# Kernel optimization log

Measured on AMD Instinct MI355X. Metric: run time of the kernel, lower is better.

## Reference

```python
import jax, jax.numpy as jnp
import numpy as np

N_LAYER = 4
N_HEAD = 16
N_EMBD = 1024
BLOCK = 1024
VOCAB = 100
TRANS = 16          # obs_dim + action_dim + 2 = 11 + 3 + 2
OBS_DIM = 11
ACT_DIM = 3
B, T = 2, 1024
VTOT = VOCAB * TRANS + 1  # token embedding rows
LN_EPS = 1e-5


def _layernorm(x, w, b):
    mu = jnp.mean(x, axis=-1, keepdims=True)
    var = jnp.var(x, axis=-1, keepdims=True)
    return (x - mu) * jax.lax.rsqrt(var + LN_EPS) * w + b


def _build_mask(t):
    # causal tril with every (joined_dim-1 mod joined_dim) column zeroed
    jd = OBS_DIM + ACT_DIM + 2  # 16
    m = jnp.tril(jnp.ones((t, t), dtype=bool))
    cols = jnp.arange(t)
    m = m & ((cols % jd) != (jd - 1))[None, :]
    return m  # [T, T] bool, True = keep


def setup_inputs() -> dict:
    key = jax.random.key(0)
    ks = jax.random.split(key, 24)
    C, L, F4 = N_EMBD, N_LAYER, 4 * N_EMBD
    g = lambda k, s: jax.random.normal(k, s, dtype=jnp.float32) * 0.02
    return {
        "tokens": jax.random.randint(ks[0], (B, T), 0, VTOT),
        "tok_emb": g(ks[1], (VTOT, C)),
        "pos_emb": g(ks[2], (1, BLOCK, C)),
        "Wq": g(ks[3], (L, C, C)), "bq": jnp.zeros((L, C), jnp.float32),
        "Wk": g(ks[4], (L, C, C)), "bk": jnp.zeros((L, C), jnp.float32),
        "Wv": g(ks[5], (L, C, C)), "bv": jnp.zeros((L, C), jnp.float32),
        "Wp": g(ks[6], (L, C, C)), "bp": jnp.zeros((L, C), jnp.float32),
        "ln1w": jnp.ones((L, C), jnp.float32), "ln1b": jnp.zeros((L, C), jnp.float32),
        "ln2w": jnp.ones((L, C), jnp.float32), "ln2b": jnp.zeros((L, C), jnp.float32),
        "W1": g(ks[7], (L, C, F4)), "b1": jnp.zeros((L, F4), jnp.float32),
        "W2": g(ks[8], (L, F4, C)), "b2": jnp.zeros((L, C), jnp.float32),
        "lnfw": jnp.ones((C,), jnp.float32), "lnfb": jnp.zeros((C,), jnp.float32),
        "head_w": g(ks[9], (TRANS, VOCAB + 1, C)),
    }


def _forward(tokens, tok_emb, pos_emb, Wq, bq, Wk, bk, Wv, bv, Wp, bp,
             ln1w, ln1b, ln2w, ln2b, W1, b1, W2, b2, lnfw, lnfb, head_w):
    b, t = tokens.shape
    C, H = N_EMBD, N_HEAD
    D = C // H
    scale = 1.0 / np.sqrt(D)
    mask = _build_mask(t)[None, None]  # [1,1,T,T]

    x = tok_emb[tokens] + pos_emb[:, :t, :]  # [B,T,C]
    for i in range(N_LAYER):
        h = _layernorm(x, ln1w[i], ln1b[i])
        q = (h @ Wq[i] + bq[i]).reshape(b, t, H, D).transpose(0, 2, 1, 3)
        k = (h @ Wk[i] + bk[i]).reshape(b, t, H, D).transpose(0, 2, 1, 3)
        v = (h @ Wv[i] + bv[i]).reshape(b, t, H, D).transpose(0, 2, 1, 3)
        att = jnp.einsum('bhtd,bhsd->bhts', q, k) * scale  # attn_bias=None => +0
        att = jnp.where(mask, att, -jnp.inf)
        att = jax.nn.softmax(att, axis=-1)
        y = jnp.einsum('bhts,bhsd->bhtd', att, v)
        y = y.transpose(0, 2, 1, 3).reshape(b, t, C)
        x = x + (y @ Wp[i] + bp[i])
        h2 = _layernorm(x, ln2w[i], ln2b[i])
        x = x + (jax.nn.gelu(h2 @ W1[i] + b1[i], approximate=False) @ W2[i] + b2[i])

    x = _layernorm(x, lnfw, lnfb)
    # pad_to_full_observation + EinLinear head
    n_pad = (TRANS - t % TRANS) % TRANS
    if n_pad:
        x = jnp.concatenate([x, jnp.zeros((b, n_pad, C), x.dtype)], axis=1)
    x_pad = x.reshape(-1, TRANS, C)                    # [b*n_states, TRANS, C]
    logits = jnp.einsum('eoi,bei->beo', head_w, x_pad)  # EinLinear, bias=False
    logits = logits.reshape(b, t + n_pad, VOCAB + 1)[:, :t]
    return logits


def reference(tokens, tok_emb, pos_emb, Wq, bq, Wk, bk, Wv, bv, Wp, bp,
              ln1w, ln1b, ln2w, ln2b, W1, b1, W2, b2, lnfw, lnfb, head_w):
    return _forward(tokens, tok_emb, pos_emb, Wq, bq, Wk, bk, Wv, bv, Wp, bp,
                    ln1w, ln1b, ln2w, ln2b, W1, b1, W2, b2, lnfw, lnfb, head_w)
```

## Files before the change

### kernel.cpp

```cpp
#include <hip/hip_runtime.h>
#include <hip/hip_bf16.h>
#include <math.h>

typedef unsigned short u16;
typedef __attribute__((ext_vector_type(8))) short short8;
typedef __attribute__((ext_vector_type(4))) float f32x4;

#define CDIM 1024
#define TDIM 1024
#define NROWS 2048
#define HEADS 16
#define HD 64
#define F4 4096

__device__ __forceinline__ u16 f2bf(float f) {
    union { float f; unsigned u; } v; v.f = f;
    unsigned r = v.u + 0x7fffu + ((v.u >> 16) & 1u);
    return (u16)(r >> 16);
}

__device__ __forceinline__ void gload_lds16(const void* g, void* lds) {
    __builtin_amdgcn_global_load_lds(
        (const __attribute__((address_space(1))) unsigned int*)g,
        (__attribute__((address_space(3))) unsigned int*)lds,
        16, 0, 0);
}

__global__ __launch_bounds__(256)
void embed_k(const int* __restrict__ tok, const float* __restrict__ te,
             const float* __restrict__ pe, float* __restrict__ X)
{
    const int row = blockIdx.x;
    const int t = row & (TDIM - 1);
    const int tk = tok[row];
    const int c = threadIdx.x * 4;
    float4 a = *reinterpret_cast<const float4*>(te + (size_t)tk * CDIM + c);
    float4 b = *reinterpret_cast<const float4*>(pe + (size_t)t * CDIM + c);
    a.x += b.x; a.y += b.y; a.z += b.z; a.w += b.w;
    *reinterpret_cast<float4*>(X + (size_t)row * CDIM + c) = a;
}

template<bool BF16OUT>
__global__ __launch_bounds__(256)
void ln_k(const float* __restrict__ X, const float* __restrict__ g,
          const float* __restrict__ be, void* __restrict__ outp)
{
    __shared__ float red[4], red2[4];
    const int row = blockIdx.x, tid = threadIdx.x;
    const float* xr = X + (size_t)row * CDIM;
    const int c = tid * 4;
    float4 xv = *reinterpret_cast<const float4*>(xr + c);
    float s  = xv.x + xv.y + xv.z + xv.w;
    float s2 = xv.x*xv.x + xv.y*xv.y + xv.z*xv.z + xv.w*xv.w;
    #pragma unroll
    for (int off = 32; off; off >>= 1) {
        s  += __shfl_xor(s, off);
        s2 += __shfl_xor(s2, off);
    }
    if ((tid & 63) == 0) { red[tid >> 6] = s; red2[tid >> 6] = s2; }
    __syncthreads();
    const float ts  = red[0] + red[1] + red[2] + red[3];
    const float ts2 = red2[0] + red2[1] + red2[2] + red2[3];
    const float mu  = ts * (1.0f / CDIM);
    const float var = ts2 * (1.0f / CDIM) - mu * mu;
    const float rs  = rsqrtf(var + 1e-5f);
    float4 gv = *reinterpret_cast<const float4*>(g + c);
    float4 bv = *reinterpret_cast<const float4*>(be + c);
    float o0 = (xv.x - mu) * rs * gv.x + bv.x;
    float o1 = (xv.y - mu) * rs * gv.y + bv.y;
    float o2 = (xv.z - mu) * rs * gv.z + bv.z;
    float o3 = (xv.w - mu) * rs * gv.w + bv.w;
    if (BF16OUT) {
        u16 tmp[4] = { f2bf(o0), f2bf(o1), f2bf(o2), f2bf(o3) };
        u16* o = (u16*)outp + (size_t)row * CDIM + c;
        *reinterpret_cast<uint2*>(o) = *reinterpret_cast<const uint2*>(tmp);
    } else {
        float4 ov = { o0, o1, o2, o3 };
        *reinterpret_cast<float4*>((float*)outp + (size_t)row * CDIM + c) = ov;
    }
}

__global__ __launch_bounds__(256)
void convT_k(const float* __restrict__ W, u16* __restrict__ Wt,
             const int K, const int N)
{
    __shared__ u16 s[64][72];
    const int k0 = blockIdx.y * 64, n0 = blockIdx.x * 64;
    const int tr = threadIdx.x >> 4, tc = (threadIdx.x & 15) * 4;
    #pragma unroll
    for (int i = 0; i < 4; ++i) {
        int r = tr + i * 16;
        float4 w = *reinterpret_cast<const float4*>(W + (size_t)(k0 + r) * N + n0 + tc);
        s[r][tc + 0] = f2bf(w.x); s[r][tc + 1] = f2bf(w.y);
        s[r][tc + 2] = f2bf(w.z); s[r][tc + 3] = f2bf(w.w);
    }
    __syncthreads();
    #pragma unroll
    for (int i = 0; i < 4; ++i) {
        int n = tr + i * 16;
        u16 tmp[4];
        #pragma unroll
        for (int e = 0; e < 4; ++e) tmp[e] = s[tc + e][n];
        *reinterpret_cast<uint2*>(Wt + (size_t)(n0 + n) * K + k0 + tc) =
            *reinterpret_cast<const uint2*>(tmp);
    }
}

template<int EPI>
__global__ __launch_bounds__(256, 2)
void gemm_bt(const u16* __restrict__ A, const u16* __restrict__ Bt,
             const float* __restrict__ bias, u16* __restrict__ outb,
             float* __restrict__ resid, u16* __restrict__ vtout,
             const int N, const int K, const int KCH)
{
    __shared__ __align__(16) u16 sA[2][2][128 * 32];
    __shared__ __align__(16) u16 sB[2][2][128 * 32];
    const int tid = threadIdx.x;
    const int lane = tid & 63, wv = tid >> 6;
    const int m0 = blockIdx.y * 128, n0 = blockIdx.x * 128;
    const int kbeg = blockIdx.z * KCH, kend = kbeg + KCH;
    const int fr = lane & 15, fq = lane >> 4;
    const int wm = wv & 1, wn = wv >> 1;
    const int srow = lane >> 2, schunk = (lane & 3) * 8;
    f32x4 acc[4][4] = {};

    auto stage = [&](int k0, int buf) {
        #pragma unroll
        for (int kk = 0; kk < 2; ++kk)
            #pragma unroll
            for (int i = 0; i < 2; ++i) {
                const int reg = i * 4 + wv;
                gload_lds16(A  + (size_t)(m0 + reg * 16 + srow) * K + k0 + kk * 32 + schunk,
                            &sA[buf][kk][reg * 512]);
                gload_lds16(Bt + (size_t)(n0 + reg * 16 + srow) * K + k0 + kk * 32 + schunk,
                            &sB[buf][kk][reg * 512]);
            }
    };

    stage(kbeg, 0);
    int cur = 0;
    for (int k0 = kbeg; k0 < kend; k0 += 64) {
        __syncthreads();
        if (k0 + 64 < kend) stage(k0 + 64, cur ^ 1);
        #pragma unroll
        for (int kk = 0; kk < 2; ++kk) {
            short8 af[4], bf[4];
            #pragma unroll
            for (int mi = 0; mi < 4; ++mi)
                af[mi] = *reinterpret_cast<const short8*>(
                    &sA[cur][kk][(wm * 64 + mi * 16 + fr) * 32 + fq * 8]);
            #pragma unroll
            for (int nj = 0; nj < 4; ++nj)
                bf[nj] = *reinterpret_cast<const short8*>(
                    &sB[cur][kk][(wn * 64 + nj * 16 + fr) * 32 + fq * 8]);
            #pragma unroll
            for (int mi = 0; mi < 4; ++mi)
                #pragma unroll
                for (int nj = 0; nj < 4; ++nj)
                    acc[mi][nj] = __builtin_amdgcn_mfma_f32_16x16x32_bf16(af[mi], bf[nj], acc[mi][nj], 0, 0, 0);
        }
        cur ^= 1;
    }

    #pragma unroll
    for (int nj = 0; nj < 4; ++nj) {
        const int col = n0 + wn * 64 + nj * 16 + fr;
        const float bias_v = (EPI == 2 && blockIdx.z != 0) ? 0.0f : bias[col];
        #pragma unroll
        for (int mi = 0; mi < 4; ++mi) {
            const int rowb = m0 + wm * 64 + mi * 16 + fq * 4;
            if (EPI == 0 && vtout != nullptr && col >= 2048) {
                const int bidx = rowb >> 10, t = rowb & 1023, hd = col - 2048;
                u16 t4[4];
                #pragma unroll
                for (int r = 0; r < 4; ++r) t4[r] = f2bf(acc[mi][nj][r] + bias_v);
                *reinterpret_cast<uint2*>(
                    vtout + ((size_t)(bidx * 16 + (hd >> 6)) * 64 + (hd & 63)) * 1024 + t) =
                    *reinterpret_cast<const uint2*>(t4);
            } else {
                #pragma unroll
                for (int r = 0; r < 4; ++r) {
                    const int row = rowb + r;
                    float cv = acc[mi][nj][r] + bias_v;
                    if (EPI == 0) {
                        outb[(size_t)row * N + col] = f2bf(cv);
                    } else if (EPI == 1) {
                        float gl = 0.5f * cv * (1.0f + erff(cv * 0.70710678118654752f));
                        outb[(size_t)row * N + col] = f2bf(gl);
                    } else {
                        atomicAdd(&resid[(size_t)row * N + col], cv);
                    }
                }
            }
        }
    }
}

__global__ __launch_bounds__(256)
void attn_k(const u16* __restrict__ QKV, const u16* __restrict__ VT,
            u16* __restrict__ Y)
{
    __shared__ __align__(16) u16 sQ[64][72];
    __shared__ __align__(16) u16 sK[2][64][72];
    __shared__ __align__(16) u16 sV[2][64][72];
    __shared__ __align__(16) u16 sP[64][72];
    const int tid = threadIdx.x, lane = tid & 63, wv = tid >> 6;
    const int fr = lane & 15, fq = lane >> 4;
    const int qt = gridDim.x - 1 - blockIdx.x;
    const int h = blockIdx.y, b = blockIdx.z, q0 = qt * 64;
    const u16* Qb = QKV + (size_t)b * TDIM * 3072 + h * HD;
    const u16* Vb = VT + ((size_t)(b * HEADS + h) * HD) * TDIM;
    const int r0 = tid >> 3, c0 = (tid & 7) * 8;

    #pragma unroll
    for (int i = 0; i < 2; ++i) {
        const int r = r0 + i * 32;
        *reinterpret_cast<uint4*>(&sQ[r][c0]) =
            *reinterpret_cast<const uint4*>(Qb + (size_t)(q0 + r) * 3072 + c0);
        *reinterpret_cast<uint4*>(&sK[0][r][c0]) =
            *reinterpret_cast<const uint4*>(Qb + 1024 + (size_t)r * 3072 + c0);
        *reinterpret_cast<uint4*>(&sV[0][r][c0]) =
            *reinterpret_cast<const uint4*>(Vb + (size_t)r * TDIM + c0);
    }
    __syncthreads();

    short8 ones;
    #pragma unroll
    for (int e = 0; e < 8; ++e) ones[e] = (short)0x3F80;

    short8 aQ0 = *reinterpret_cast<const short8*>(&sQ[wv * 16 + fr][fq * 8]);
    short8 aQ1 = *reinterpret_cast<const short8*>(&sQ[wv * 16 + fr][32 + fq * 8]);
    f32x4 o[4] = {};
    f32x4 osum = {};

    for (int st = 0; st <= qt; ++st) {
        const int cur = st & 1, s0 = st * 64;
        const bool pf = st < qt;
        uint4 pk[2], pv[2];
        if (pf) {
            #pragma unroll
            for (int i = 0; i < 2; ++i) {
                const int r = r0 + i * 32;
                pk[i] = *reinterpret_cast<const uint4*>(Qb + 1024 + (size_t)(s0 + 64 + r) * 3072 + c0);
                pv[i] = *reinterpret_cast<const uint4*>(Vb + (size_t)r * TDIM + s0 + 64 + c0);
            }
        }
        f32x4 sacc[4] = {};
        #pragma unroll
        for (int j = 0; j < 4; ++j) {
            short8 b0 = *reinterpret_cast<const short8*>(&sK[cur][j * 16 + fr][fq * 8]);
            sacc[j] = __builtin_amdgcn_mfma_f32_16x16x32_bf16(aQ0, b0, sacc[j], 0, 0, 0);
            short8 b1 = *reinterpret_cast<const short8*>(&sK[cur][j * 16 + fr][32 + fq * 8]);
            sacc[j] = __builtin_amdgcn_mfma_f32_16x16x32_bf16(aQ1, b1, sacc[j], 0, 0, 0);
        }
        #pragma unroll
        for (int j = 0; j < 4; ++j)
            #pragma unroll
            for (int r = 0; r < 4; ++r) {
                const int qrow = q0 + wv * 16 + fq * 4 + r;
                const int scol = s0 + j * 16 + fr;
                const bool keep = (scol <= qrow) && ((scol & 15) != 15);
                const float p = keep ? __expf(sacc[j][r] * 0.125f) : 0.0f;
                sP[wv * 16 + fq * 4 + r][j * 16 + fr] = f2bf(p);
            }
        short8 aP0 = *reinterpret_cast<const short8*>(&sP[wv * 16 + fr][fq * 8]);
        short8 aP1 = *reinterpret_cast<const short8*>(&sP[wv * 16 + fr][32 + fq * 8]);
        #pragma unroll
        for (int j = 0; j < 4; ++j) {
            short8 b0 = *reinterpret_cast<const short8*>(&sV[cur][j * 16 + fr][fq * 8]);
            o[j] = __builtin_amdgcn_mfma_f32_16x16x32_bf16(aP0, b0, o[j], 0, 0, 0);
            short8 b1 = *reinterpret_cast<const short8*>(&sV[cur][j * 16 + fr][32 + fq * 8]);
            o[j] = __builtin_amdgcn_mfma_f32_16x16x32_bf16(aP1, b1, o[j], 0, 0, 0);
        }
        osum = __builtin_amdgcn_mfma_f32_16x16x32_bf16(aP0, ones, osum, 0, 0, 0);
        osum = __builtin_amdgcn_mfma_f32_16x16x32_bf16(aP1, ones, osum, 0, 0, 0);
        if (pf) {
            #pragma unroll
            for (int i = 0; i < 2; ++i) {
                const int r = r0 + i * 32;
                *reinterpret_cast<uint4*>(&sK[cur ^ 1][r][c0]) = pk[i];
                *reinterpret_cast<uint4*>(&sV[cur ^ 1][r][c0]) = pv[i];
            }
        }
        __syncthreads();
    }

    float rcp[4];
    #pragma unroll
    for (int r = 0; r < 4; ++r) rcp[r] = 1.0f / osum[r];
    const size_t ybase = ((size_t)b * TDIM + q0) * CDIM + h * HD;
    #pragma unroll
    for (int j = 0; j < 4; ++j)
        #pragma unroll
        for (int r = 0; r < 4; ++r) {
            const int row = wv * 16 + fq * 4 + r, col = j * 16 + fr;
            Y[ybase + (size_t)row * CDIM + col] = f2bf(o[j][r] * rcp[r]);
        }
}

__global__ __launch_bounds__(256)
void head_k(const float* __restrict__ Xf, const float* __restrict__ HW,
             float* __restrict__ out)
{
    const int row = blockIdx.x;
    const int e = row & 15;
    const float* xr = Xf + (size_t)row * CDIM;
    const float* wbase = HW + (size_t)e * 101 * CDIM;
    const int lane = threadIdx.x & 63, wv = threadIdx.x >> 6;
    for (int o = wv; o < 101; o += 4) {
        const float* wr = wbase + (size_t)o * CDIM;
        float s = 0.0f;
        #pragma unroll
        for (int i = 0; i < CDIM / 64; ++i)
            s += xr[lane + i * 64] * wr[lane + i * 64];
        #pragma unroll
        for (int off = 32; off; off >>= 1) s += __shfl_xor(s, off);
        if (lane == 0) out[(size_t)row * 101 + o] = s;
    }
}

extern "C" void kernel_launch(void* const* d_in, const int* in_sizes, int n_in,
                              void* d_out, int out_size, void* d_ws, size_t ws_size,
                              hipStream_t stream)
{
    const int*   tokens = (const int*)  d_in[0];
    const float* tok_emb= (const float*)d_in[1];
    const float* pos_emb= (const float*)d_in[2];
    const float* Wq = (const float*)d_in[3];
    const float* bq = (const float*)d_in[4];
    const float* Wk = (const float*)d_in[5];
    const float* bk = (const float*)d_in[6];
    const float* Wv = (const float*)d_in[7];
    const float* bv = (const float*)d_in[8];
    const float* Wp = (const float*)d_in[9];
    const float* bp = (const float*)d_in[10];
    const float* ln1w = (const float*)d_in[11];
    const float* ln1b = (const float*)d_in[12];
    const float* ln2w = (const float*)d_in[13];
    const float* ln2b = (const float*)d_in[14];
    const float* W1 = (const float*)d_in[15];
    const float* b1 = (const float*)d_in[16];
    const float* W2 = (const float*)d_in[17];
    const float* b2 = (const float*)d_in[18];
    const float* lnfw = (const float*)d_in[19];
    const float* lnfb = (const float*)d_in[20];
    const float* head_w = (const float*)d_in[21];
    float* out = (float*)d_out;

    char* ws = (char*)d_ws;
    float* x    = (float*)(ws);
    u16*   hbuf = (u16*)  (ws + (8u  << 20));
    u16*   yb   = (u16*)  (ws + (8u  << 20));
    u16*   qkv  = (u16*)  (ws + (12u << 20));
    u16*   vt   = (u16*)  (ws + (24u << 20));
    u16*   mid  = (u16*)  (ws + (12u << 20));
    float* hf   = (float*)(ws + (12u << 20));
    u16*   wbuf = (u16*)  (ws + (28u << 20));
    float* bbuf = (float*)(ws + (36u << 20));

    embed_k<<<NROWS, 256, 0, stream>>>(tokens, tok_emb, pos_emb, x);

    for (int l = 0; l < 4; ++l) {
        const size_t wo = (size_t)l * CDIM * CDIM;
        convT_k<<<dim3(16, 16), 256, 0, stream>>>(Wq + wo, wbuf + 0u * CDIM * CDIM, CDIM, CDIM);
        convT_k<<<dim3(16, 16), 256, 0, stream>>>(Wk + wo, wbuf + 1u * CDIM * CDIM, CDIM, CDIM);
        convT_k<<<dim3(16, 16), 256, 0, stream>>>(Wv + wo, wbuf + 2u * CDIM * CDIM, CDIM, CDIM);
        hipMemcpyAsync(bbuf,        bq + l * CDIM, CDIM * 4, hipMemcpyDeviceToDevice, stream);
        hipMemcpyAsync(bbuf + 1024, bk + l * CDIM, CDIM * 4, hipMemcpyDeviceToDevice, stream);
        hipMemcpyAsync(bbuf + 2048, bv + l * CDIM, CDIM * 4, hipMemcpyDeviceToDevice, stream);

        ln_k<true><<<NROWS, 256, 0, stream>>>(x, ln1w + l * CDIM, ln1b + l * CDIM, hbuf);
        gemm_bt<0><<<dim3(24, 16, 1), 256, 0, stream>>>(hbuf, wbuf, bbuf, qkv, nullptr, vt, 3072, CDIM, CDIM);
        attn_k<<<dim3(16, HEADS, 2), 256, 0, stream>>>(qkv, vt, yb);

        convT_k<<<dim3(16, 16), 256, 0, stream>>>(Wp + wo, wbuf, CDIM, CDIM);
        gemm_bt<2><<<dim3(8, 16, 2), 256, 0, stream>>>(yb, wbuf, bp + l * CDIM, nullptr, x, nullptr, CDIM, CDIM, 512);

        ln_k<true><<<NROWS, 256, 0, stream>>>(x, ln2w + l * CDIM, ln2b + l * CDIM, hbuf);
        convT_k<<<dim3(64, 16), 256, 0, stream>>>(W1 + (size_t)l * CDIM * F4, wbuf, CDIM, F4);
        gemm_bt<1><<<dim3(32, 16, 1), 256, 0, stream>>>(hbuf, wbuf, b1 + l * F4, mid, nullptr, nullptr, F4, CDIM, CDIM);
        convT_k<<<dim3(16, 64), 256, 0, stream>>>(W2 + (size_t)l * F4 * CDIM, wbuf, F4, CDIM);
        gemm_bt<2><<<dim3(8, 16, 4), 256, 0, stream>>>(mid, wbuf, b2 + l * CDIM, nullptr, x, nullptr, CDIM, F4, CDIM);
    }

    ln_k<false><<<NROWS, 256, 0, stream>>>(x, lnfw, lnfb, hf);
    head_k<<<NROWS, 256, 0, stream>>>(hf, head_w, out);
}
```

Measured before the change: 1.083 ms.

## Remap GEMM and attention workgroups per XCD with grouped tile order; pack biases in kernel

Adds a tile_map helper that turns the linear workgroup id into tile coordinates. Consecutive tiles land on the same XCD, and M tiles are grouped in bands of 8, which should improve L2 reuse of A and B panels on the MI355X's multi-die layout. The mapping is applied to the GEMM and attention kernels. The three device-to-device hipMemcpyAsync calls per layer for the QKV biases are replaced with a single small kernel to cut launch overhead. The remap adds some integer arithmetic per block and changes the order in which causal attention tiles are scheduled.

New measurement: 1.060 ms. -2.1%, faster.

```diff
diff --git a/kernel.cpp b/kernel.cpp
--- a/kernel.cpp
+++ b/kernel.cpp
@@ -24,6 +24,27 @@
         (const __attribute__((address_space(1))) unsigned int*)g,
         (__attribute__((address_space(3))) unsigned int*)lds,
         16, 0, 0);
+}
+
+__device__ __forceinline__ void tile_map(int& bx, int& by, int& bz)
+{
+    const int gx = gridDim.x, gy = gridDim.y;
+    const int fid = blockIdx.x + gx * (blockIdx.y + gy * blockIdx.z);
+    const int nwg = gx * gy * gridDim.z;
+    const int q = nwg >> 3, r = nwg & 7;
+    const int xcd = fid & 7, t = fid >> 3;
+    const int n = ((xcd < r) ? xcd * (q + 1) : r * (q + 1) + (xcd - r) * q) + t;
+    const int nxy = gx * gy;
+    bz = n / nxy;
+    const int xy = n - bz * nxy;
+    const int per_group = gx << 3;
+    const int grp = xy / per_group;
+    const int in = xy - grp * per_group;
+    const int y0 = grp << 3;
+    const int rem = gy - y0;
+    const int gh = rem < 8 ? rem : 8;
+    by = y0 + (in % gh);
+    bx = in / gh;
 }
 
 __global__ __launch_bounds__(256)
@@ -106,6 +127,16 @@
     }
 }
 
+__global__ __launch_bounds__(256)
+void pack_bias_k(const float* __restrict__ a, const float* __restrict__ b,
+                 const float* __restrict__ c, float* __restrict__ o)
+{
+    const int i = threadIdx.x * 4;
+    const float* s = blockIdx.x == 0 ? a : blockIdx.x == 1 ? b : c;
+    *reinterpret_cast<float4*>(o + (size_t)blockIdx.x * 1024 + i) =
+        *reinterpret_cast<const float4*>(s + i);
+}
+
 template<int EPI>
 __global__ __launch_bounds__(256, 2)
 void gemm_bt(const u16* __restrict__ A, const u16* __restrict__ Bt,
@@ -117,8 +148,10 @@
     __shared__ __align__(16) u16 sB[2][2][128 * 32];
     const int tid = threadIdx.x;
     const int lane = tid & 63, wv = tid >> 6;
-    const int m0 = blockIdx.y * 128, n0 = blockIdx.x * 128;
-    const int kbeg = blockIdx.z * KCH, kend = kbeg + KCH;
+    int bx, by, bz;
+    tile_map(bx, by, bz);
+    const int m0 = by * 128, n0 = bx * 128;
+    const int kbeg = bz * KCH, kend = kbeg + KCH;
     const int fr = lane & 15, fq = lane >> 4;
     const int wm = wv & 1, wn = wv >> 1;
     const int srow = lane >> 2, schunk = (lane & 3) * 8;
@@ -165,7 +198,7 @@
     #pragma unroll
     for (int nj = 0; nj < 4; ++nj) {
         const int col = n0 + wn * 64 + nj * 16 + fr;
-        const float bias_v = (EPI == 2 && blockIdx.z != 0) ? 0.0f : bias[col];
+        const float bias_v = (EPI == 2 && bz != 0) ? 0.0f : bias[col];
         #pragma unroll
         for (int mi = 0; mi < 4; ++mi) {
             const int rowb = m0 + wm * 64 + mi * 16 + fq * 4;
@@ -206,8 +239,10 @@
     __shared__ __align__(16) u16 sP[64][72];
     const int tid = threadIdx.x, lane = tid & 63, wv = tid >> 6;
     const int fr = lane & 15, fq = lane >> 4;
-    const int qt = gridDim.x - 1 - blockIdx.x;
-    const int h = blockIdx.y, b = blockIdx.z, q0 = qt * 64;
+    int bx, by, bz;
+    tile_map(bx, by, bz);
+    const int qt = gridDim.x - 1 - bx;
+    const int h = by, b = bz, q0 = qt * 64;
     const u16* Qb = QKV + (size_t)b * TDIM * 3072 + h * HD;
     const u16* Vb = VT + ((size_t)(b * HEADS + h) * HD) * TDIM;
     const int r0 = tid >> 3, c0 = (tid & 7) * 8;
@@ -365,9 +400,7 @@
         convT_k<<<dim3(16, 16), 256, 0, stream>>>(Wq + wo, wbuf + 0u * CDIM * CDIM, CDIM, CDIM);
         convT_k<<<dim3(16, 16), 256, 0, stream>>>(Wk + wo, wbuf + 1u * CDIM * CDIM, CDIM, CDIM);
         convT_k<<<dim3(16, 16), 256, 0, stream>>>(Wv + wo, wbuf + 2u * CDIM * CDIM, CDIM, CDIM);
-        hipMemcpyAsync(bbuf,        bq + l * CDIM, CDIM * 4, hipMemcpyDeviceToDevice, stream);
-        hipMemcpyAsync(bbuf + 1024, bk + l * CDIM, CDIM * 4, hipMemcpyDeviceToDevice, stream);
-        hipMemcpyAsync(bbuf + 2048, bv + l * CDIM, CDIM * 4, hipMemcpyDeviceToDevice, stream);
+        pack_bias_k<<<3, 256, 0, stream>>>(bq + l * CDIM, bk + l * CDIM, bv + l * CDIM, bbuf);
 
         ln_k<true><<<NROWS, 256, 0, stream>>>(x, ln1w + l * CDIM, ln1b + l * CDIM, hbuf);
         gemm_bt<0><<<dim3(24, 16, 1), 256, 0, stream>>>(hbuf, wbuf, bbuf, qkv, nullptr, vt, 3072, CDIM, CDIM);
```
